# Performance work log

Measured on AMD Instinct MI355X. Metric: run time of the kernel, lower is better.

The kernel has to match this reference:

```python
import jax, jax.numpy as jnp
import numpy as np
from jax import lax

B, N, NPOINT, NSAMPLE, D = 16, 8192, 1024, 32, 64
MLP = [64, 64, 128]
IN_CH = 3 + D
EPS = 1e-5


def farthest_point_sample(xyz, npoint):
    # xyz: [B, N, 3]; deterministic start at index 0 (torch uses randint start)
    b, n, _ = xyz.shape

    def step(carry, _):
        distance, farthest = carry
        centroid = jnp.take_along_axis(xyz, farthest[:, None, None], axis=1)  # [B,1,3]
        dist = jnp.sum((xyz - centroid) ** 2, axis=-1)  # [B,N]
        distance = jnp.minimum(distance, dist)
        nxt = jnp.argmax(distance, axis=-1).astype(jnp.int32)
        return (distance, nxt), farthest

    init = (jnp.full((b, n), 1e10, dtype=xyz.dtype), jnp.zeros((b,), dtype=jnp.int32))
    _, idxs = lax.scan(step, init, None, length=npoint)
    return idxs.T  # [B, npoint]


def knn_idx(k, xyz, new_xyz):
    # squared distances via expansion (avoids [B,S,N,3] intermediate)
    d = (jnp.sum(new_xyz ** 2, -1)[:, :, None]
         + jnp.sum(xyz ** 2, -1)[:, None, :]
         - 2.0 * jnp.einsum('bsc,bnc->bsn', new_xyz, xyz))  # [B,S,N]
    return lax.top_k(-d, k)[1]  # [B,S,k] indices of k smallest


def gather_points(points, idx):
    # points: [B,N,C], idx: [B,S,K] -> [B,S,K,C]
    return jax.vmap(lambda p, i: p[i])(points, idx)


def setup_inputs():
    key = jax.random.key(0)
    ks = jax.random.split(key, 2 + 2 * len(MLP))
    inp = {
        'xyz': jax.random.normal(ks[0], (B, 3, N), dtype=jnp.float32),
        'points': jax.random.normal(ks[1], (B, D, N), dtype=jnp.float32),
    }
    last = IN_CH
    for li, oc in enumerate(MLP):
        inp[f'W{li}'] = jax.random.normal(ks[2 + 2 * li], (oc, last), dtype=jnp.float32) / np.sqrt(last)
        inp[f'b{li}'] = jnp.zeros((oc,), dtype=jnp.float32)
        inp[f'g{li}'] = jnp.ones((oc,), dtype=jnp.float32)
        inp[f'be{li}'] = jnp.zeros((oc,), dtype=jnp.float32)
        last = oc
    return inp


def _forward(xyz, points, params):
    xyz_t = jnp.transpose(xyz, (0, 2, 1))      # [B,N,3]
    pts_t = jnp.transpose(points, (0, 2, 1))   # [B,N,D]
    fps_idx = farthest_point_sample(xyz_t, NPOINT)               # [B,S]
    new_xyz = jnp.take_along_axis(xyz_t, fps_idx[:, :, None], 1)  # [B,S,3]
    idx = knn_idx(NSAMPLE, xyz_t, new_xyz)                        # [B,S,K]
    grouped_xyz = gather_points(xyz_t, idx)                       # [B,S,K,3]
    grouped_pts = gather_points(pts_t, idx)                       # [B,S,K,D]
    x = jnp.concatenate([grouped_xyz - new_xyz[:, :, None, :], grouped_pts], -1)  # [B,S,K,3+D]
    for (W, b, g, be) in params:
        x = jnp.einsum('bskc,oc->bsko', x, W) + b  # 1x1 conv
        mu = jnp.mean(x, axis=(0, 1, 2))           # BN (training-mode batch stats)
        var = jnp.var(x, axis=(0, 1, 2))
        x = jax.nn.relu(g * (x - mu) / jnp.sqrt(var + EPS) + be)
    new_points = jnp.max(x, axis=2)  # max over nsample -> [B,S,C]
    return jnp.transpose(new_xyz, (0, 2, 1)), jnp.transpose(new_points, (0, 2, 1))


def reference(xyz, points, W0, b0, g0, be0, W1, b1, g1, be1, W2, b2, g2, be2):
    params = [(W0, b0, g0, be0), (W1, b1, g1, be1), (W2, b2, g2, be2)]
    return _forward(xyz, points, params)
```

## Files before the change

### kernel.cpp

```cpp
#include <hip/hip_runtime.h>
#include <stdint.h>

#define B_    16
#define N_    8192
#define S_    1024
#define K_    32
#define D_    64
#define CIN   67
#define C1    64
#define C3    128
#define FSTR  68
#define NP_   (B_*S_*K_)
#define EPS_  1e-5f
#define FPT   512

typedef unsigned long long u64;
typedef unsigned int u32;

__device__ __forceinline__ u32 fmap(float f) {
  u32 u = __float_as_uint(f);
  u32 m = (u32)(((int)u) >> 31) | 0x80000000u;
  return u ^ m;
}

__global__ __launch_bounds__(256) void feat_kernel(const float* __restrict__ xyz,
    const float* __restrict__ pts, float* __restrict__ feat, float* __restrict__ pp) {
  __shared__ float T[128*69];
  int b  = blockIdx.x >> 6;
  int n0 = (blockIdx.x & 63) * 128;
  int tid = threadIdx.x;
  for (int e = tid; e < CIN*128; e += 256) {
    int c = e >> 7, i = e & 127;
    float v = (c < 3) ? xyz[(size_t)(b*3 + c)*N_ + n0 + i]
                      : pts[(size_t)(b*D_ + (c-3))*N_ + n0 + i];
    T[i*69 + c] = v;
  }
  __syncthreads();
  for (int e = tid; e < 128*FSTR; e += 256) {
    int i = e / FSTR, c = e - i*FSTR;
    float v = (c < CIN) ? T[i*69 + c] : 0.f;
    feat[((size_t)(b*N_ + n0 + i))*FSTR + c] = v;
  }
  if (tid < 128) {
    float x = T[tid*69+0], y = T[tid*69+1], z = T[tid*69+2];
    pp[(size_t)b*N_ + n0 + tid] =
      __fadd_rn(__fadd_rn(__fmul_rn(x,x), __fmul_rn(y,y)), __fmul_rn(z,z));
  }
}

__global__ __launch_bounds__(FPT) void fps_kernel(const float* __restrict__ xyz,
    float* __restrict__ nxyz, float* __restrict__ qq, float* __restrict__ out0) {
  __shared__ float sx[N_], sy[N_], sz[N_];
  __shared__ u64 lk[2][FPT/64];
  __shared__ int hist[S_];
  int b = blockIdx.x, tid = threadIdx.x;
  float px[16], py[16], pz[16], dist[16];
#pragma unroll
  for (int j = 0; j < 16; ++j) {
    int n = j*FPT + tid;
    float x = xyz[(size_t)(b*3+0)*N_ + n];
    float y = xyz[(size_t)(b*3+1)*N_ + n];
    float z = xyz[(size_t)(b*3+2)*N_ + n];
    px[j] = x; py[j] = y; pz[j] = z;
    sx[n] = x; sy[n] = y; sz[n] = z;
    dist[j] = 1e10f;
  }
  if (tid == 0) hist[0] = 0;
  __syncthreads();
  float cx = sx[0], cy = sy[0], cz = sz[0];
  int wid = tid >> 6, lane = tid & 63;
  for (int t = 1; t < S_; ++t) {
    float bv = -1.f; int bn = 0;
#pragma unroll
    for (int j = 0; j < 16; ++j) {
      float dx = __fsub_rn(px[j], cx), dy = __fsub_rn(py[j], cy), dz = __fsub_rn(pz[j], cz);
      float d = __fadd_rn(__fadd_rn(__fmul_rn(dx,dx), __fmul_rn(dy,dy)), __fmul_rn(dz,dz));
      float nd = fminf(dist[j], d);
      dist[j] = nd;
      bool gt = nd > bv;
      bv = gt ? nd : bv;
      bn = gt ? (j*FPT + tid) : bn;
    }
    u64 best = ((u64)__float_as_uint(bv) << 32) | (u32)(N_-1 - bn);
#pragma unroll
    for (int off = 32; off > 0; off >>= 1) {
      u64 o = __shfl_xor((unsigned long long)best, off, 64);
      best = o > best ? o : best;
    }
    if (lane == 0) lk[t & 1][wid] = best;
    __syncthreads();
    u64 M = lk[t & 1][0];
#pragma unroll
    for (int w = 1; w < FPT/64; ++w) { u64 o = lk[t & 1][w]; M = o > M ? o : M; }
    int cur = N_-1 - (int)(u32)(M & 0xFFFFFFFFu);
    cx = sx[cur]; cy = sy[cur]; cz = sz[cur];
    if (tid == 0) hist[t] = cur;
  }
  __syncthreads();
  for (int s = tid; s < S_; s += FPT) {
    int n = hist[s];
    float x = sx[n], y = sy[n], z = sz[n];
    nxyz[(size_t)(b*S_ + s)*3 + 0] = x;
    nxyz[(size_t)(b*S_ + s)*3 + 1] = y;
    nxyz[(size_t)(b*S_ + s)*3 + 2] = z;
    qq[(size_t)b*S_ + s] =
      __fadd_rn(__fadd_rn(__fmul_rn(x,x), __fmul_rn(y,y)), __fmul_rn(z,z));
    out0[(size_t)(b*3+0)*S_ + s] = x;
    out0[(size_t)(b*3+1)*S_ + s] = y;
    out0[(size_t)(b*3+2)*S_ + s] = z;
  }
}

__global__ __launch_bounds__(256) void knn_kernel(const float* __restrict__ xyz,
    const float* __restrict__ pp, const float* __restrict__ nxyz,
    const float* __restrict__ qq, int* __restrict__ knn_out) {
  __shared__ u64 lk[2][4];
  __shared__ u32 outl[K_];
  int q = blockIdx.x;
  int b = q >> 10;
  int tid = threadIdx.x;
  float qx = nxyz[(size_t)q*3+0], qy = nxyz[(size_t)q*3+1], qz = nxyz[(size_t)q*3+2];
  float qv = qq[q];
  u64 key[32];
#pragma unroll
  for (int j = 0; j < 32; ++j) {
    int n = j*256 + tid;
    float px = xyz[(size_t)(b*3+0)*N_ + n];
    float py = xyz[(size_t)(b*3+1)*N_ + n];
    float pz = xyz[(size_t)(b*3+2)*N_ + n];
    float dot = __fadd_rn(__fadd_rn(__fmul_rn(qx,px), __fmul_rn(qy,py)), __fmul_rn(qz,pz));
    float d = __fsub_rn(__fadd_rn(qv, pp[(size_t)b*N_ + n]), __fmul_rn(2.0f, dot));
    key[j] = ((u64)fmap(d) << 32) | (u32)n;
  }
  u64 cm = key[0];
#pragma unroll
  for (int j = 1; j < 32; ++j) cm = key[j] < cm ? key[j] : cm;
  int wid = tid >> 6, lane = tid & 63;
  for (int r = 0; r < K_; ++r) {
    u64 v = cm;
#pragma unroll
    for (int off = 32; off > 0; off >>= 1) {
      u64 o = __shfl_xor((unsigned long long)v, off, 64);
      v = o < v ? o : v;
    }
    if (lane == 0) lk[r & 1][wid] = v;
    __syncthreads();
    u64 M = lk[r & 1][0];
#pragma unroll
    for (int w = 1; w < 4; ++w) { u64 o = lk[r & 1][w]; M = o < M ? o : M; }
    if (tid == 0) outl[r] = (u32)(M & 0xFFFFFFFFu);
    if (cm == M) {
#pragma unroll
      for (int j = 0; j < 32; ++j) key[j] = (key[j] == M) ? ~0ull : key[j];
      u64 m2 = key[0];
#pragma unroll
      for (int j = 1; j < 32; ++j) m2 = key[j] < m2 ? key[j] : m2;
      cm = m2;
    }
  }
  __syncthreads();
  if (tid < K_) knn_out[(size_t)q*K_ + tid] = (int)outl[tid];
}

__global__ __launch_bounds__(256) void l1_kernel(const float* __restrict__ feat,
    const float* __restrict__ nxyz, const int* __restrict__ knn_in,
    const float* __restrict__ W, const float* __restrict__ bias,
    float* __restrict__ z, float* __restrict__ part) {
  __shared__ float fT[FSTR*FSTR];
  __shared__ float WT[CIN*C1];
  __shared__ float sst[2][4][C1];
  int p0 = blockIdx.x * 64, tid = threadIdx.x;
  for (int i = tid; i < C1*CIN; i += 256) {
    int o = i / CIN, c = i - o*CIN;
    WT[c*C1 + o] = W[i];
  }
  {
    int i = tid >> 2, c4 = tid & 3;
    int p = p0 + i;
    int n = knn_in[p];
    int b = p >> 15;
    int bs = p >> 5;
    size_t base = ((size_t)(b*N_ + n))*FSTR;
    float qx = nxyz[(size_t)bs*3+0], qy = nxyz[(size_t)bs*3+1], qz = nxyz[(size_t)bs*3+2];
    for (int c4i = c4; c4i < 17; c4i += 4) {
      float4 v = *(const float4*)&feat[base + (size_t)c4i*4];
      if (c4i == 0) {
        v.x = __fsub_rn(v.x, qx); v.y = __fsub_rn(v.y, qy); v.z = __fsub_rn(v.z, qz);
      }
      int c = c4i*4;
      fT[(c+0)*FSTR + i] = v.x;
      fT[(c+1)*FSTR + i] = v.y;
      fT[(c+2)*FSTR + i] = v.z;
      fT[(c+3)*FSTR + i] = v.w;
    }
  }
  __syncthreads();
  int o = tid & 63, pg = tid >> 6, pb = pg*16;
  float acc[16];
  float bv = bias[o];
#pragma unroll
  for (int i = 0; i < 16; ++i) acc[i] = bv;
  for (int k = 0; k < CIN; ++k) {
    float w = WT[k*C1 + o];
#pragma unroll
    for (int i4 = 0; i4 < 4; ++i4) {
      float4 f = *(const float4*)&fT[k*FSTR + pb + i4*4];
      acc[i4*4+0] = fmaf(w, f.x, acc[i4*4+0]);
      acc[i4*4+1] = fmaf(w, f.y, acc[i4*4+1]);
      acc[i4*4+2] = fmaf(w, f.z, acc[i4*4+2]);
      acc[i4*4+3] = fmaf(w, f.w, acc[i4*4+3]);
    }
  }
  float s1 = 0.f, s2 = 0.f;
#pragma unroll
  for (int i = 0; i < 16; ++i) {
    int p = p0 + pb + i;
    z[(size_t)p*C1 + o] = acc[i];
    s1 = __fadd_rn(s1, acc[i]);
    s2 = fmaf(acc[i], acc[i], s2);
  }
  sst[0][pg][o] = s1; sst[1][pg][o] = s2;
  __syncthreads();
  if (tid < C1) {
    float a = ((sst[0][0][tid] + sst[0][1][tid]) + sst[0][2][tid]) + sst[0][3][tid];
    float c = ((sst[1][0][tid] + sst[1][1][tid]) + sst[1][2][tid]) + sst[1][3][tid];
    part[(size_t)blockIdx.x*(2*C1) + tid]      = a;
    part[(size_t)blockIdx.x*(2*C1) + C1 + tid] = c;
  }
}

__global__ __launch_bounds__(256) void l2_kernel(float* __restrict__ z,
    const float* __restrict__ W, const float* __restrict__ bias,
    const float* __restrict__ scale, const float* __restrict__ shift,
    float* __restrict__ part) {
  __shared__ float fT[C1*FSTR];
  __shared__ float WT[C1*C1];
  __shared__ float sst[2][4][C1];
  __shared__ float sc[C1], sh[C1];
  int p0 = blockIdx.x * 64, tid = threadIdx.x;
  if (tid < C1) { sc[tid] = scale[tid]; sh[tid] = shift[tid]; }
  for (int i = tid; i < C1*C1; i += 256) {
    int o = i >> 6, c = i & 63;
    WT[c*C1 + o] = W[i];
  }
  __syncthreads();
  {
    int i = tid >> 2, c4 = tid & 3;
    const float4* zrow = (const float4*)&z[(size_t)(p0+i)*C1];
#pragma unroll
    for (int it = 0; it < 4; ++it) {
      int c4i = c4 + it*4;
      float4 v = zrow[c4i];
      int c = c4i*4;
      fT[(c+0)*FSTR + i] = fmaxf(0.f, fmaf(v.x, sc[c+0], sh[c+0]));
      fT[(c+1)*FSTR + i] = fmaxf(0.f, fmaf(v.y, sc[c+1], sh[c+1]));
      fT[(c+2)*FSTR + i] = fmaxf(0.f, fmaf(v.z, sc[c+2], sh[c+2]));
      fT[(c+3)*FSTR + i] = fmaxf(0.f, fmaf(v.w, sc[c+3], sh[c+3]));
    }
  }
  __syncthreads();
  int o = tid & 63, pg = tid >> 6, pb = pg*16;
  float acc[16];
  float bv = bias[o];
#pragma unroll
  for (int i = 0; i < 16; ++i) acc[i] = bv;
  for (int k = 0; k < C1; ++k) {
    float w = WT[k*C1 + o];
#pragma unroll
    for (int i4 = 0; i4 < 4; ++i4) {
      float4 f = *(const float4*)&fT[k*FSTR + pb + i4*4];
      acc[i4*4+0] = fmaf(w, f.x, acc[i4*4+0]);
      acc[i4*4+1] = fmaf(w, f.y, acc[i4*4+1]);
      acc[i4*4+2] = fmaf(w, f.z, acc[i4*4+2]);
      acc[i4*4+3] = fmaf(w, f.w, acc[i4*4+3]);
    }
  }
  float s1 = 0.f, s2 = 0.f;
#pragma unroll
  for (int i = 0; i < 16; ++i) {
    int p = p0 + pb + i;
    z[(size_t)p*C1 + o] = acc[i];
    s1 = __fadd_rn(s1, acc[i]);
    s2 = fmaf(acc[i], acc[i], s2);
  }
  sst[0][pg][o] = s1; sst[1][pg][o] = s2;
  __syncthreads();
  if (tid < C1) {
    float a = ((sst[0][0][tid] + sst[0][1][tid]) + sst[0][2][tid]) + sst[0][3][tid];
    float c = ((sst[1][0][tid] + sst[1][1][tid]) + sst[1][2][tid]) + sst[1][3][tid];
    part[(size_t)blockIdx.x*(2*C1) + tid]      = a;
    part[(size_t)blockIdx.x*(2*C1) + C1 + tid] = c;
  }
}

__global__ __launch_bounds__(256) void l3_kernel(const float* __restrict__ z,
    const float* __restrict__ W, const float* __restrict__ bias,
    const float* __restrict__ scale, const float* __restrict__ shift,
    float* __restrict__ pmax, float* __restrict__ pmin, float* __restrict__ part) {
  __shared__ float fT[C1*FSTR];
  __shared__ float WT[C1*C3];
  __shared__ float sst[2][2][C3];
  __shared__ float sc[C1], sh[C1];
  int p0 = blockIdx.x * 64, tid = threadIdx.x;
  if (tid < C1) { sc[tid] = scale[tid]; sh[tid] = shift[tid]; }
  for (int i = tid; i < C3*C1; i += 256) {
    int o = i >> 6, c = i & 63;
    WT[c*C3 + o] = W[i];
  }
  __syncthreads();
  {
    int i = tid >> 2, c4 = tid & 3;
    const float4* zrow = (const float4*)&z[(size_t)(p0+i)*C1];
#pragma unroll
    for (int it = 0; it < 4; ++it) {
      int c4i = c4 + it*4;
      float4 v = zrow[c4i];
      int c = c4i*4;
      fT[(c+0)*FSTR + i] = fmaxf(0.f, fmaf(v.x, sc[c+0], sh[c+0]));
      fT[(c+1)*FSTR + i] = fmaxf(0.f, fmaf(v.y, sc[c+1], sh[c+1]));
      fT[(c+2)*FSTR + i] = fmaxf(0.f, fmaf(v.z, sc[c+2], sh[c+2]));
      fT[(c+3)*FSTR + i] = fmaxf(0.f, fmaf(v.w, sc[c+3], sh[c+3]));
    }
  }
  __syncthreads();
  int o = tid & 127, g = tid >> 7, pb = g*32;
  float acc[32];
  float bv = bias[o];
#pragma unroll
  for (int i = 0; i < 32; ++i) acc[i] = bv;
  for (int k = 0; k < C1; ++k) {
    float w = WT[k*C3 + o];
#pragma unroll
    for (int i4 = 0; i4 < 8; ++i4) {
      float4 f = *(const float4*)&fT[k*FSTR + pb + i4*4];
      acc[i4*4+0] = fmaf(w, f.x, acc[i4*4+0]);
      acc[i4*4+1] = fmaf(w, f.y, acc[i4*4+1]);
      acc[i4*4+2] = fmaf(w, f.z, acc[i4*4+2]);
      acc[i4*4+3] = fmaf(w, f.w, acc[i4*4+3]);
    }
  }
  float mx = acc[0], mn = acc[0], s1 = 0.f, s2 = 0.f;
#pragma unroll
  for (int i = 0; i < 32; ++i) {
    mx = fmaxf(mx, acc[i]);
    mn = fminf(mn, acc[i]);
    s1 = __fadd_rn(s1, acc[i]);
    s2 = fmaf(acc[i], acc[i], s2);
  }
  int bs = (p0 >> 5) + g;
  pmax[(size_t)bs*C3 + o] = mx;
  pmin[(size_t)bs*C3 + o] = mn;
  sst[0][g][o] = s1; sst[1][g][o] = s2;
  __syncthreads();
  if (tid < C3) {
    part[(size_t)blockIdx.x*(2*C3) + tid]      = sst[0][0][tid] + sst[0][1][tid];
    part[(size_t)blockIdx.x*(2*C3) + C3 + tid] = sst[1][0][tid] + sst[1][1][tid];
  }
}

template<int C>
__global__ __launch_bounds__(256) void red_kernel(const float* __restrict__ part,
    int nblk, const float* __restrict__ g, const float* __restrict__ be,
    float* __restrict__ scale, float* __restrict__ shift) {
  __shared__ float r1[256], r2[256];
  int o = blockIdx.x, tid = threadIdx.x;
  float s1 = 0.f, s2 = 0.f;
  for (int j = tid; j < nblk; j += 256) {
    s1 += part[(size_t)j*(2*C) + o];
    s2 += part[(size_t)j*(2*C) + C + o];
  }
  r1[tid] = s1; r2[tid] = s2;
  __syncthreads();
  for (int off = 128; off > 0; off >>= 1) {
    if (tid < off) { r1[tid] += r1[tid+off]; r2[tid] += r2[tid+off]; }
    __syncthreads();
  }
  if (tid == 0) {
    float cnt = (float)NP_;
    float mean = r1[0] / cnt;
    float var  = fmaxf(r2[0] / cnt - mean*mean, 0.f);
    float s = g[o] / sqrtf(var + EPS_);
    scale[o] = s;
    shift[o] = be[o] - mean * s;
  }
}

__global__ __launch_bounds__(256) void final_kernel(const float* __restrict__ pmax,
    const float* __restrict__ pmin, const float* __restrict__ scale,
    const float* __restrict__ shift, float* __restrict__ out1) {
  int i = blockIdx.x*256 + threadIdx.x;
  if (i >= B_*C3*S_) return;
  int s = i & 1023;
  int o = (i >> 10) & 127;
  int b = i >> 17;
  int bs = b*S_ + s;
  float sc = scale[o], sh = shift[o];
  float v = (sc >= 0.f) ? pmax[(size_t)bs*C3 + o] : pmin[(size_t)bs*C3 + o];
  out1[i] = fmaxf(0.f, __fadd_rn(__fmul_rn(v, sc), sh));
}

extern "C" void kernel_launch(void* const* d_in, const int* in_sizes, int n_in,
                              void* d_out, int out_size, void* d_ws, size_t ws_size,
                              hipStream_t stream) {
  const float* xyz = (const float*)d_in[0];
  const float* pts = (const float*)d_in[1];
  const float* W0  = (const float*)d_in[2];
  const float* b0  = (const float*)d_in[3];
  const float* g0  = (const float*)d_in[4];
  const float* be0 = (const float*)d_in[5];
  const float* W1  = (const float*)d_in[6];
  const float* b1  = (const float*)d_in[7];
  const float* g1  = (const float*)d_in[8];
  const float* be1 = (const float*)d_in[9];
  const float* W2  = (const float*)d_in[10];
  const float* b2  = (const float*)d_in[11];
  const float* g2  = (const float*)d_in[12];
  const float* be2 = (const float*)d_in[13];

  float* ws = (float*)d_ws;
  size_t off = 0;
  float* feat = ws + off;  off += (size_t)B_*N_*FSTR;
  float* pp   = ws + off;  off += (size_t)B_*N_;
  float* nxyz = ws + off;  off += (size_t)B_*S_*3;
  float* qq   = ws + off;  off += (size_t)B_*S_;
  int*   knn  = (int*)(ws + off); off += (size_t)B_*S_*K_;
  float* z    = ws + off;  off += (size_t)NP_*C1;
  float* part1 = ws + off; off += (size_t)8192*2*C1;
  float* part2 = ws + off; off += (size_t)8192*2*C1;
  float* part3 = ws + off; off += (size_t)8192*2*C3;
  float* pmax = ws + off;  off += (size_t)B_*S_*C3;
  float* pmin = ws + off;  off += (size_t)B_*S_*C3;
  float* sc1 = ws + off; off += C1;  float* sh1 = ws + off; off += C1;
  float* sc2 = ws + off; off += C1;  float* sh2 = ws + off; off += C1;
  float* sc3 = ws + off; off += C3;  float* sh3 = ws + off; off += C3;
  (void)ws_size; (void)in_sizes; (void)n_in; (void)out_size;

  float* out0 = (float*)d_out;
  float* out1 = out0 + (size_t)B_*3*S_;

  feat_kernel<<<dim3(B_*64), dim3(256), 0, stream>>>(xyz, pts, feat, pp);
  fps_kernel<<<dim3(B_), dim3(FPT), 0, stream>>>(xyz, nxyz, qq, out0);
  knn_kernel<<<dim3(B_*S_), dim3(256), 0, stream>>>(xyz, pp, nxyz, qq, knn);
  l1_kernel<<<dim3(NP_/64), dim3(256), 0, stream>>>(feat, nxyz, knn, W0, b0, z, part1);
  red_kernel<C1><<<dim3(C1), dim3(256), 0, stream>>>(part1, NP_/64, g0, be0, sc1, sh1);
  l2_kernel<<<dim3(NP_/64), dim3(256), 0, stream>>>(z, W1, b1, sc1, sh1, part2);
  red_kernel<C1><<<dim3(C1), dim3(256), 0, stream>>>(part2, NP_/64, g1, be1, sc2, sh2);
  l3_kernel<<<dim3(NP_/64), dim3(256), 0, stream>>>(z, W2, b2, sc2, sh2, pmax, pmin, part3);
  red_kernel<C3><<<dim3(C3), dim3(256), 0, stream>>>(part3, NP_/64, g2, be2, sc3, sh3);
  final_kernel<<<dim3((B_*C3*S_ + 255)/256), dim3(256), 0, stream>>>(pmax, pmin, sc3, sh3, out1);
}
```

Measured before the change: 2.385 ms.

## Restructure KNN top-k with per-wave DPP reductions and a final 8-way merge

The KNN kernel now uses 512 threads with 16 keys each instead of 256 threads with 32 keys. Each wave independently extracts its own 32 smallest keys using DPP row/broadcast min steps plus readlane, so the per-round block-wide __syncthreads is gone. One thread then merges the eight sorted per-wave lists into the final top-32. This removes 32 block barriers and shuffle-based reductions per query. In exchange it adds a serial 32-step merge on a single thread, and it relies on DPP broadcast controls (0x142/0x143) that must behave correctly on the target wave64 hardware.

After: 2.684 ms. 12.5% more time.

```diff
diff --git a/kernel.cpp b/kernel.cpp
--- a/kernel.cpp
+++ b/kernel.cpp
@@ -13,6 +13,8 @@
 #define NP_   (B_*S_*K_)
 #define EPS_  1e-5f
 #define FPT   512
+#define KNT   512
+#define KPT   16
 
 typedef unsigned long long u64;
 typedef unsigned int u32;
@@ -111,20 +113,30 @@
   }
 }
 
-__global__ __launch_bounds__(256) void knn_kernel(const float* __restrict__ xyz,
+#define DPP_MIN_STEP(CTRL)                                                     \
+  {                                                                            \
+    int tv = __builtin_amdgcn_update_dpp(vv, vv, CTRL, 0xF, 0xF, false);       \
+    int ti = __builtin_amdgcn_update_dpp(vi, vi, CTRL, 0xF, 0xF, false);       \
+    bool take = ((u32)tv < (u32)vv) || ((tv == vv) && ((u32)ti < (u32)vi));    \
+    vv = take ? tv : vv;                                                       \
+    vi = take ? ti : vi;                                                       \
+  }
+
+__global__ __launch_bounds__(KNT) void knn_kernel(const float* __restrict__ xyz,
     const float* __restrict__ pp, const float* __restrict__ nxyz,
     const float* __restrict__ qq, int* __restrict__ knn_out) {
-  __shared__ u64 lk[2][4];
-  __shared__ u32 outl[K_];
+  __shared__ u64 wl[8][K_];
+  __shared__ u32 obuf[K_];
   int q = blockIdx.x;
   int b = q >> 10;
   int tid = threadIdx.x;
+  int wid = tid >> 6, lane = tid & 63;
   float qx = nxyz[(size_t)q*3+0], qy = nxyz[(size_t)q*3+1], qz = nxyz[(size_t)q*3+2];
   float qv = qq[q];
-  u64 key[32];
-#pragma unroll
-  for (int j = 0; j < 32; ++j) {
-    int n = j*256 + tid;
+  u64 key[KPT];
+#pragma unroll
+  for (int j = 0; j < KPT; ++j) {
+    int n = j*KNT + tid;
     float px = xyz[(size_t)(b*3+0)*N_ + n];
     float py = xyz[(size_t)(b*3+1)*N_ + n];
     float pz = xyz[(size_t)(b*3+2)*N_ + n];
@@ -134,32 +146,56 @@
   }
   u64 cm = key[0];
 #pragma unroll
-  for (int j = 1; j < 32; ++j) cm = key[j] < cm ? key[j] : cm;
-  int wid = tid >> 6, lane = tid & 63;
+  for (int j = 1; j < KPT; ++j) cm = key[j] < cm ? key[j] : cm;
   for (int r = 0; r < K_; ++r) {
-    u64 v = cm;
-#pragma unroll
-    for (int off = 32; off > 0; off >>= 1) {
-      u64 o = __shfl_xor((unsigned long long)v, off, 64);
-      v = o < v ? o : v;
-    }
-    if (lane == 0) lk[r & 1][wid] = v;
-    __syncthreads();
-    u64 M = lk[r & 1][0];
-#pragma unroll
-    for (int w = 1; w < 4; ++w) { u64 o = lk[r & 1][w]; M = o < M ? o : M; }
-    if (tid == 0) outl[r] = (u32)(M & 0xFFFFFFFFu);
+    int vv = (int)(u32)(cm >> 32);
+    int vi = (int)(u32)(cm & 0xFFFFFFFFu);
+    DPP_MIN_STEP(0x111);
+    DPP_MIN_STEP(0x112);
+    DPP_MIN_STEP(0x114);
+    DPP_MIN_STEP(0x118);
+    DPP_MIN_STEP(0x142);
+    DPP_MIN_STEP(0x143);
+    int Mv = __builtin_amdgcn_readlane(vv, 63);
+    int Mi = __builtin_amdgcn_readlane(vi, 63);
+    u64 M = ((u64)(u32)Mv << 32) | (u32)Mi;
+    if (lane == 0) wl[wid][r] = M;
     if (cm == M) {
-#pragma unroll
-      for (int j = 0; j < 32; ++j) key[j] = (key[j] == M) ? ~0ull : key[j];
-      u64 m2 = key[0];
-#pragma unroll
-      for (int j = 1; j < 32; ++j) m2 = key[j] < m2 ? key[j] : m2;
-      cm = m2;
-    }
-  }
-  __syncthreads();
-  if (tid < K_) knn_out[(size_t)q*K_ + tid] = (int)outl[tid];
+      u64 nm = ~0ull;
+#pragma unroll
+      for (int j = 0; j < KPT; ++j) {
+        u64 k2 = key[j];
+        k2 = (k2 == M) ? ~0ull : k2;
+        key[j] = k2;
+        nm = k2 < nm ? k2 : nm;
+      }
+      cm = nm;
+    }
+  }
+  __syncthreads();
+  if (tid == 0) {
+    u64 h0 = wl[0][0], h1 = wl[1][0], h2 = wl[2][0], h3 = wl[3][0];
+    u64 h4 = wl[4][0], h5 = wl[5][0], h6 = wl[6][0], h7 = wl[7][0];
+    int p0 = 1, p1 = 1, p2 = 1, p3 = 1, p4 = 1, p5 = 1, p6 = 1, p7 = 1;
+    for (int i = 0; i < K_; ++i) {
+      u64 m01 = h0 < h1 ? h0 : h1;  int i01 = h0 < h1 ? 0 : 1;
+      u64 m23 = h2 < h3 ? h2 : h3;  int i23 = h2 < h3 ? 2 : 3;
+      u64 m45 = h4 < h5 ? h4 : h5;  int i45 = h4 < h5 ? 4 : 5;
+      u64 m67 = h6 < h7 ? h6 : h7;  int i67 = h6 < h7 ? 6 : 7;
+      u64 m03 = m01 < m23 ? m01 : m23;  int i03 = m01 < m23 ? i01 : i23;
+      u64 m47 = m45 < m67 ? m45 : m67;  int i47 = m45 < m67 ? i45 : i67;
+      u64 mv  = m03 < m47 ? m03 : m47;  int mi  = m03 < m47 ? i03 : i47;
+      obuf[i] = (u32)(mv & 0xFFFFFFFFu);
+      int np = (mi==0)?p0:(mi==1)?p1:(mi==2)?p2:(mi==3)?p3:(mi==4)?p4:(mi==5)?p5:(mi==6)?p6:p7;
+      u64 nv = (np < K_) ? wl[mi][np] : ~0ull;
+      p0 += (mi==0); p1 += (mi==1); p2 += (mi==2); p3 += (mi==3);
+      p4 += (mi==4); p5 += (mi==5); p6 += (mi==6); p7 += (mi==7);
+      h0 = (mi==0)?nv:h0; h1 = (mi==1)?nv:h1; h2 = (mi==2)?nv:h2; h3 = (mi==3)?nv:h3;
+      h4 = (mi==4)?nv:h4; h5 = (mi==5)?nv:h5; h6 = (mi==6)?nv:h6; h7 = (mi==7)?nv:h7;
+    }
+  }
+  __syncthreads();
+  if (tid < K_) knn_out[(size_t)q*K_ + tid] = (int)obuf[tid];
 }
 
 __global__ __launch_bounds__(256) void l1_kernel(const float* __restrict__ feat,
@@ -440,7 +476,7 @@
 
   feat_kernel<<<dim3(B_*64), dim3(256), 0, stream>>>(xyz, pts, feat, pp);
   fps_kernel<<<dim3(B_), dim3(FPT), 0, stream>>>(xyz, nxyz, qq, out0);
-  knn_kernel<<<dim3(B_*S_), dim3(256), 0, stream>>>(xyz, pp, nxyz, qq, knn);
+  knn_kernel<<<dim3(B_*S_), dim3(KNT), 0, stream>>>(xyz, pp, nxyz, qq, knn);
   l1_kernel<<<dim3(NP_/64), dim3(256), 0, stream>>>(feat, nxyz, knn, W0, b0, z, part1);
   red_kernel<C1><<<dim3(C1), dim3(256), 0, stream>>>(part1, NP_/64, g0, be0, sc1, sh1);
   l2_kernel<<<dim3(NP_/64), dim3(256), 0, stream>>>(z, W1, b1, sc1, sh1, part2);
```
